# Optimization experiments

Hardware: AMD Instinct MI355X
Metric: run time of the kernel (lower is better)

## Reference

```python
import jax, jax.numpy as jnp
import numpy as np


def setup_inputs() -> dict:
    key = jax.random.key(0)
    k1, k2, k3, k4 = jax.random.split(key, 4)
    batch, d_in, d_out, K, M = 4096, 1024, 1024, 16, 512
    x = jax.random.normal(k1, (batch, d_in), dtype=jnp.float32)
    A = jax.random.normal(k2, (K, d_in, M), dtype=jnp.float32) * (1.0 / np.sqrt(d_in))
    B = jax.random.normal(k3, (K, M, d_out), dtype=jnp.float32) * (1.0 / np.sqrt(M))
    bias = jnp.zeros((d_out,), dtype=jnp.float32)
    topk_mask = jax.random.randint(k4, (batch, K), 0, 2) > 0
    return {"x": x, "topk_mask": topk_mask, "A": A, "B": B, "bias": bias}


def reference(x, topk_mask, A, B, bias):
    # pre_inner_acts: [batch, k, m]
    pre = jnp.einsum('bi,kim->bkm', x, A)
    maskf = topk_mask.astype(pre.dtype)[:, :, None]  # [batch, k, 1]
    pre = pre * maskf
    # inner_acts: [batch, k, out]
    inner_acts = jnp.einsum('bkm,kmh->bkh', pre, B)
    inner_acts = inner_acts * maskf
    out = jnp.sum(inner_acts, axis=1) + bias  # [batch, out]
    return out, inner_acts
```

## Files before the change

### kernel.cpp

```cpp
#include <hip/hip_runtime.h>

typedef __attribute__((ext_vector_type(8))) short bf16x8;
typedef __attribute__((ext_vector_type(4))) float f32x4;
typedef __attribute__((ext_vector_type(8))) unsigned short u16x8;

__device__ __forceinline__ unsigned short f2bf(float f) {
  union { float f; unsigned u; } v; v.f = f;
  unsigned r = v.u + 0x7fffu + ((v.u >> 16) & 1u);
  return (unsigned short)(r >> 16);
}

__global__ __launch_bounds__(256)
void prep_kernel(const float* __restrict__ x, unsigned short* __restrict__ x_bf,
                 const float* __restrict__ A, unsigned short* __restrict__ A_t,
                 const float* __restrict__ B, unsigned short* __restrict__ B_t,
                 const int* __restrict__ mask, int* __restrict__ rows,
                 int* __restrict__ counts) {
  __shared__ float tbuf[64][65];
  __shared__ int cnt, mcnt;
  const int bid = blockIdx.x;
  const int t = threadIdx.x;

  if (bid < 2048) {
    int slot = bid * 256 + t;
    f32x4 v0 = __builtin_nontemporal_load((const f32x4*)x + 2 * slot);
    f32x4 v1 = __builtin_nontemporal_load((const f32x4*)x + 2 * slot + 1);
    u16x8 o;
    o[0] = f2bf(v0[0]); o[1] = f2bf(v0[1]); o[2] = f2bf(v0[2]); o[3] = f2bf(v0[3]);
    o[4] = f2bf(v1[0]); o[5] = f2bf(v1[1]); o[6] = f2bf(v1[2]); o[7] = f2bf(v1[3]);
    ((u16x8*)x_bf)[slot] = o;
    return;
  }
  if (bid < 6144) {
    const float* in; unsigned short* out; int R, C, cx, ry, z;
    if (bid < 4096) {
      int idx = bid - 2048; z = idx >> 7; int local = idx & 127;
      R = 1024; C = 512; cx = local & 7; ry = local >> 3;
      in = A; out = A_t;
    } else {
      int idx = bid - 4096; z = idx >> 7; int local = idx & 127;
      R = 512; C = 1024; cx = local & 15; ry = local >> 4;
      in = B; out = B_t;
    }
    size_t eo = (size_t)z * R * C;
    const float* src = in + eo;
    unsigned short* dst = out + eo;
    int c0 = cx * 64, r0 = ry * 64;
    int tx = t & 63, ty = t >> 6;
#pragma unroll
    for (int i = 0; i < 64; i += 4)
      tbuf[ty + i][tx] = __builtin_nontemporal_load(&src[(size_t)(r0 + ty + i) * C + (c0 + tx)]);
    __syncthreads();
#pragma unroll
    for (int i = 0; i < 64; i += 4)
      dst[(size_t)(c0 + ty + i) * R + (r0 + tx)] = f2bf(tbuf[tx][ty + i]);
    return;
  }
  {
    int z = bid - 6144;
    if (t == 0) { cnt = 0; mcnt = 0; }
    __syncthreads();
    int* rz = rows + (size_t)z * 4096;
    for (int i = t; i < 4096; i += 256) {
      bool m = mask[(size_t)i * 16 + z] != 0;
      unsigned long long bal = __ballot(m);
      int lane = t & 63;
      int pa = __popcll(bal & ((1ull << lane) - 1ull));
      int ta = __popcll(bal);
      int base_a, base_m;
      if (lane == 0) { base_a = atomicAdd(&cnt, ta); base_m = atomicAdd(&mcnt, 64 - ta); }
      base_a = __shfl(base_a, 0);
      base_m = __shfl(base_m, 0);
      int pm = lane - pa;
      if (m) rz[base_a + pa] = i;
      else   rz[4095 - (base_m + pm)] = i;
    }
    __syncthreads();
    if (t == 0) counts[z] = cnt;
  }
}

__device__ __forceinline__ void stage_tile(const unsigned short* __restrict__ src,
                                           size_t row_stride, int row0, int k0,
                                           unsigned short* lds) {
  int t = threadIdx.x;
  int lane = t & 63;
  int w = t >> 6;
#pragma unroll
  for (int i = 0; i < 4; ++i) {
    int chunk = w * 4 + i;
    int row = chunk * 8 + (lane >> 3);
    int glog = (lane & 7) ^ (row & 7);
    const unsigned short* g = src + (size_t)(row0 + row) * row_stride + (size_t)(k0 + glog * 8);
    __builtin_amdgcn_global_load_lds((const __attribute__((address_space(1))) unsigned int*)g,
                                     (__attribute__((address_space(3))) unsigned int*)(lds + chunk * 512),
                                     16, 0, 0);
  }
}

__device__ __forceinline__ bf16x8 read_frag(const unsigned short* lds, int row, int gb) {
  int phys = (row * 128 + gb) ^ ((row & 7) << 4);
  return *(const bf16x8*)((const char*)lds + phys);
}

__global__ __launch_bounds__(256)
void gemm1_kernel(const unsigned short* __restrict__ X,
                  const unsigned short* __restrict__ W,
                  unsigned short* __restrict__ pre_out,
                  const int* __restrict__ rows,
                  const int* __restrict__ counts) {
  const int gx = gridDim.x, gy = gridDim.y;
  int lin = blockIdx.x + gx * (blockIdx.y + gy * blockIdx.z);
  int cpx = (gx * gy * gridDim.z) >> 3;
  lin = (lin & 7) * cpx + (lin >> 3);
  int bx = lin % gx; lin /= gx;
  int by = lin % gy; lin /= gy;
  const int z = lin;
  const int cnt = counts[z];
  const int tb = by * 128;
  const int tn = bx * 128;
  const int t = threadIdx.x;

  if (tb >= cnt) return;

  __shared__ unsigned short Xs[128 * 64];
  __shared__ unsigned short Ws[128 * 64];
  __shared__ int rowsS[128];

  if (t < 128) rowsS[t] = rows[(size_t)z * 4096 + tb + t];
  __syncthreads();

  const int lane = t & 63;
  const int wv = t >> 6;
  const int wr = (wv >> 1) * 64;
  const int wc = (wv & 1) * 64;
  const int fr = lane & 15;
  const int fg = lane >> 4;

  const unsigned short* Wbase = W + (size_t)z * 512 * 1024;

  int xoff[4];
#pragma unroll
  for (int i = 0; i < 4; ++i) {
    int chunk = wv * 4 + i;
    int row = chunk * 8 + (lane >> 3);
    int glog = (lane & 7) ^ (row & 7);
    xoff[i] = rowsS[row] * 1024 + glog * 8;
  }

  f32x4 acc[4][4] = {};

  for (int kt = 0; kt < 16; ++kt) {
    if (kt) __syncthreads();
    {
      const int k64 = kt * 64;
#pragma unroll
      for (int i = 0; i < 4; ++i) {
        int chunk = wv * 4 + i;
        __builtin_amdgcn_global_load_lds(
            (const __attribute__((address_space(1))) unsigned int*)(X + xoff[i] + k64),
            (__attribute__((address_space(3))) unsigned int*)(Xs + chunk * 512), 16, 0, 0);
      }
    }
    stage_tile(Wbase, 1024, tn, kt * 64, Ws);
    __syncthreads();
#pragma unroll
    for (int kk = 0; kk < 2; ++kk) {
      const int gb = kk * 64 + fg * 16;
      bf16x8 xf[4], wf[4];
#pragma unroll
      for (int i = 0; i < 4; ++i) {
        xf[i] = read_frag(Xs, wr + i * 16 + fr, gb);
        wf[i] = read_frag(Ws, wc + i * 16 + fr, gb);
      }
#pragma unroll
      for (int mi = 0; mi < 4; ++mi)
#pragma unroll
        for (int ni = 0; ni < 4; ++ni)
          acc[mi][ni] = __builtin_amdgcn_mfma_f32_16x16x32_bf16(xf[mi], wf[ni], acc[mi][ni], 0, 0, 0);
    }
  }

#pragma unroll
  for (int mi = 0; mi < 4; ++mi) {
#pragma unroll
    for (int j = 0; j < 4; ++j) {
      int rl = wr + mi * 16 + fg * 4 + j;
      size_t rowbase = (size_t)z * 4096 * 512 + (size_t)(tb + rl) * 512;
#pragma unroll
      for (int ni = 0; ni < 4; ++ni) {
        int m = tn + wc + ni * 16 + fr;
        pre_out[rowbase + m] = f2bf(acc[mi][ni][j]);
      }
    }
  }
}

__global__ __launch_bounds__(256)
void gemm2_kernel(const unsigned short* __restrict__ X,
                  const unsigned short* __restrict__ W,
                  float* __restrict__ inner_out,
                  const int* __restrict__ rows,
                  const int* __restrict__ counts) {
  const int gx = gridDim.x, gy = gridDim.y;
  int lin = blockIdx.x + gx * (blockIdx.y + gy * blockIdx.z);
  int cpx = (gx * gy * gridDim.z) >> 3;
  lin = (lin & 7) * cpx + (lin >> 3);
  int bx = lin % gx; lin /= gx;
  int by = lin % gy; lin /= gy;
  const int z = lin;
  const int cnt = counts[z];
  const int tb = by * 128;
  const int tn = bx * 128;
  const int t = threadIdx.x;

  __shared__ unsigned short Xs[128 * 64];
  __shared__ unsigned short Ws[128 * 64];
  __shared__ int rowsS[128];

  if (t < 128) rowsS[t] = rows[(size_t)z * 4096 + tb + t];
  __syncthreads();

  if (tb >= cnt) {
    const f32x4 z4 = {0.f, 0.f, 0.f, 0.f};
#pragma unroll
    for (int it = 0; it < 16; ++it) {
      int rl = it * 8 + (t >> 5);
      int b = rowsS[rl];
      f32x4* p = (f32x4*)(inner_out + (size_t)b * (16 * 1024) + (size_t)z * 1024 + tn) + (t & 31);
      __builtin_nontemporal_store(z4, p);
    }
    return;
  }

  const int lane = t & 63;
  const int wv = t >> 6;
  const int wr = (wv >> 1) * 64;
  const int wc = (wv & 1) * 64;
  const int fr = lane & 15;
  const int fg = lane >> 4;

  const unsigned short* Xbase = X + (size_t)z * 4096 * 512;
  const unsigned short* Wbase = W + (size_t)z * 1024 * 512;

  f32x4 acc[4][4] = {};

  for (int kt = 0; kt < 8; ++kt) {
    if (kt) __syncthreads();
    stage_tile(Xbase, 512, tb, kt * 64, Xs);
    stage_tile(Wbase, 512, tn, kt * 64, Ws);
    __syncthreads();
#pragma unroll
    for (int kk = 0; kk < 2; ++kk) {
      const int gb = kk * 64 + fg * 16;
      bf16x8 xf[4], wf[4];
#pragma unroll
      for (int i = 0; i < 4; ++i) {
        xf[i] = read_frag(Xs, wr + i * 16 + fr, gb);
        wf[i] = read_frag(Ws, wc + i * 16 + fr, gb);
      }
#pragma unroll
      for (int mi = 0; mi < 4; ++mi)
#pragma unroll
        for (int ni = 0; ni < 4; ++ni)
          acc[mi][ni] = __builtin_amdgcn_mfma_f32_16x16x32_bf16(xf[mi], wf[ni], acc[mi][ni], 0, 0, 0);
    }
  }

#pragma unroll
  for (int mi = 0; mi < 4; ++mi) {
#pragma unroll
    for (int j = 0; j < 4; ++j) {
      int rl = wr + mi * 16 + fg * 4 + j;
      int b = rowsS[rl];
      size_t rowbase = (size_t)b * (16 * 1024) + (size_t)z * 1024;
      if (tb + rl < cnt) {
#pragma unroll
        for (int ni = 0; ni < 4; ++ni) {
          int h = tn + wc + ni * 16 + fr;
          inner_out[rowbase + h] = acc[mi][ni][j];
        }
      } else {
#pragma unroll
        for (int ni = 0; ni < 4; ++ni) {
          int h = tn + wc + ni * 16 + fr;
          __builtin_nontemporal_store(0.f, &inner_out[rowbase + h]);
        }
      }
    }
  }
}

__global__ __launch_bounds__(256)
void reduce_kernel(const float* __restrict__ inner, const float* __restrict__ bias,
                   const int* __restrict__ mask, float* __restrict__ out) {
  int b = blockIdx.x;
  int t = threadIdx.x;
  __shared__ int mrow[16];
  if (t < 16) mrow[t] = mask[(size_t)b * 16 + t];
  __syncthreads();
  f32x4 bv = *((const f32x4*)bias + t);
  f32x4 s = bv;
  const f32x4* ip = (const f32x4*)(inner + (size_t)b * (16 * 1024)) + t;
#pragma unroll
  for (int k = 0; k < 16; ++k) {
    if (mrow[k]) {
      f32x4 v = __builtin_nontemporal_load(ip + (size_t)k * 256);
      s += v;
    }
  }
  __builtin_nontemporal_store(s, (f32x4*)out + (size_t)b * 256 + t);
}

extern "C" void kernel_launch(void* const* d_in, const int* in_sizes, int n_in,
                              void* d_out, int out_size, void* d_ws, size_t ws_size,
                              hipStream_t stream) {
  const float* x    = (const float*)d_in[0];
  const int*   mask = (const int*)d_in[1];
  const float* A    = (const float*)d_in[2];
  const float* B    = (const float*)d_in[3];
  const float* bias = (const float*)d_in[4];

  float* out   = (float*)d_out;
  float* inner = (float*)d_out + (size_t)4096 * 1024;

  if (ws_size < 109314112ull) return;
  char* ws = (char*)d_ws;
  unsigned short* x_bf = (unsigned short*)ws;
  unsigned short* A_t  = (unsigned short*)(ws + ((size_t)8 << 20));
  unsigned short* B_t  = (unsigned short*)(ws + ((size_t)24 << 20));
  unsigned short* pre  = (unsigned short*)(ws + ((size_t)40 << 20));
  int* rows            = (int*)(ws + ((size_t)104 << 20));
  int* counts          = (int*)(ws + ((size_t)104 << 20) + 262144);

  prep_kernel<<<6160, 256, 0, stream>>>(x, x_bf, A, A_t, B, B_t, mask, rows, counts);

  gemm1_kernel<<<dim3(4, 32, 16), 256, 0, stream>>>(x_bf, A_t, pre, rows, counts);
  gemm2_kernel<<<dim3(8, 32, 16), 256, 0, stream>>>(pre, B_t, inner, rows, counts);

  reduce_kernel<<<4096, 256, 0, stream>>>(inner, bias, mask, out);
}
```

Measured before the change: 167.2 us.

## Move zero-fill of masked inner_acts rows from gemm2 into gemm1 side blocks

Zeroing the inner_acts rows for masked-out (batch, expert) pairs moves out of gemm2's tail tiles. gemm1 is now launched on a 1D grid with 2048 extra blocks that write those zeros with nontemporal stores while the GEMM blocks run. gemm2 only handles active rows, so its partial tiles no longer write zeros and its fully inactive tiles exit early. The aim is to overlap the zero-fill's memory traffic with gemm1's compute and to trim gemm2's store work, at the cost of extra tiny blocks and a hand-built block-to-tile mapping in gemm1.

New measurement: 164.2 us (median of 2 runs). No clear change (-1.8%).

```diff
diff --git a/kernel.cpp b/kernel.cpp
--- a/kernel.cpp
+++ b/kernel.cpp
@@ -107,20 +107,41 @@
 void gemm1_kernel(const unsigned short* __restrict__ X,
                   const unsigned short* __restrict__ W,
                   unsigned short* __restrict__ pre_out,
+                  float* __restrict__ inner_out,
                   const int* __restrict__ rows,
                   const int* __restrict__ counts) {
-  const int gx = gridDim.x, gy = gridDim.y;
-  int lin = blockIdx.x + gx * (blockIdx.y + gy * blockIdx.z);
-  int cpx = (gx * gy * gridDim.z) >> 3;
-  lin = (lin & 7) * cpx + (lin >> 3);
-  int bx = lin % gx; lin /= gx;
-  int by = lin % gy; lin /= gy;
-  const int z = lin;
+  const int o = blockIdx.x;
+  const int chunk = o & 7;
+  const int pos = o >> 3;
+  const int t = threadIdx.x;
+
+  if (pos >= 256) {
+    int w = chunk * 256 + (pos - 256);
+    int z = w >> 7;
+    int sub = w & 127;
+    int cnt = counts[z];
+    int slot0 = cnt + sub * 32;
+    if (slot0 >= 4096) return;
+    const int* rz = rows + (size_t)z * 4096;
+    const f32x4 z4 = {0.f, 0.f, 0.f, 0.f};
+#pragma unroll 4
+    for (int i = 0; i < 32; ++i) {
+      int slot = slot0 + i;
+      if (slot >= 4096) break;
+      int b = rz[slot];
+      f32x4* p = (f32x4*)(inner_out + (size_t)b * (16 * 1024) + (size_t)z * 1024) + t;
+      __builtin_nontemporal_store(z4, p);
+    }
+    return;
+  }
+
+  int g = chunk * 256 + pos;
+  const int bx = g & 3;
+  const int by = (g >> 2) & 31;
+  const int z = g >> 7;
   const int cnt = counts[z];
   const int tb = by * 128;
   const int tn = bx * 128;
-  const int t = threadIdx.x;
-
   if (tb >= cnt) return;
 
   __shared__ unsigned short Xs[128 * 64];
@@ -142,8 +163,8 @@
   int xoff[4];
 #pragma unroll
   for (int i = 0; i < 4; ++i) {
-    int chunk = wv * 4 + i;
-    int row = chunk * 8 + (lane >> 3);
+    int chnk = wv * 4 + i;
+    int row = chnk * 8 + (lane >> 3);
     int glog = (lane & 7) ^ (row & 7);
     xoff[i] = rowsS[row] * 1024 + glog * 8;
   }
@@ -156,10 +177,10 @@
       const int k64 = kt * 64;
 #pragma unroll
       for (int i = 0; i < 4; ++i) {
-        int chunk = wv * 4 + i;
+        int chnk = wv * 4 + i;
         __builtin_amdgcn_global_load_lds(
             (const __attribute__((address_space(1))) unsigned int*)(X + xoff[i] + k64),
-            (__attribute__((address_space(3))) unsigned int*)(Xs + chunk * 512), 16, 0, 0);
+            (__attribute__((address_space(3))) unsigned int*)(Xs + chnk * 512), 16, 0, 0);
       }
     }
     stage_tile(Wbase, 1024, tn, kt * 64, Ws);
@@ -214,24 +235,14 @@
   const int tn = bx * 128;
   const int t = threadIdx.x;
 
+  if (tb >= cnt) return;
+
   __shared__ unsigned short Xs[128 * 64];
   __shared__ unsigned short Ws[128 * 64];
   __shared__ int rowsS[128];
 
   if (t < 128) rowsS[t] = rows[(size_t)z * 4096 + tb + t];
   __syncthreads();
-
-  if (tb >= cnt) {
-    const f32x4 z4 = {0.f, 0.f, 0.f, 0.f};
-#pragma unroll
-    for (int it = 0; it < 16; ++it) {
-      int rl = it * 8 + (t >> 5);
-      int b = rowsS[rl];
-      f32x4* p = (f32x4*)(inner_out + (size_t)b * (16 * 1024) + (size_t)z * 1024 + tn) + (t & 31);
-      __builtin_nontemporal_store(z4, p);
-    }
-    return;
-  }
 
   const int lane = t & 63;
   const int wv = t >> 6;
@@ -272,19 +283,13 @@
 #pragma unroll
     for (int j = 0; j < 4; ++j) {
       int rl = wr + mi * 16 + fg * 4 + j;
-      int b = rowsS[rl];
-      size_t rowbase = (size_t)b * (16 * 1024) + (size_t)z * 1024;
       if (tb + rl < cnt) {
+        int b = rowsS[rl];
+        size_t rowbase = (size_t)b * (16 * 1024) + (size_t)z * 1024;
 #pragma unroll
         for (int ni = 0; ni < 4; ++ni) {
           int h = tn + wc + ni * 16 + fr;
           inner_out[rowbase + h] = acc[mi][ni][j];
-        }
-      } else {
-#pragma unroll
-        for (int ni = 0; ni < 4; ++ni) {
-          int h = tn + wc + ni * 16 + fr;
-          __builtin_nontemporal_store(0.f, &inner_out[rowbase + h]);
         }
       }
     }
@@ -335,7 +340,7 @@
 
   prep_kernel<<<6160, 256, 0, stream>>>(x, x_bf, A, A_t, B, B_t, mask, rows, counts);
 
-  gemm1_kernel<<<dim3(4, 32, 16), 256, 0, stream>>>(x_bf, A_t, pre, rows, counts);
+  gemm1_kernel<<<4096, 256, 0, stream>>>(x_bf, A_t, pre, inner, rows, counts);
   gemm2_kernel<<<dim3(8, 32, 16), 256, 0, stream>>>(pre, B_t, inner, rows, counts);
 
   reduce_kernel<<<4096, 256, 0, stream>>>(inner, bias, mask, out);
```
